# Kernel optimization log

Hardware: AMD Instinct MI355X
Metric: run time of the kernel (lower is better)

The kernel has to match this reference:

```python
import jax, jax.numpy as jnp
import numpy as np

C = 256

def setup_inputs() -> dict:
    key = jax.random.key(0)
    ks = jax.random.split(key, 7)
    s = 1.0 / np.sqrt(C)
    x = jax.random.normal(ks[0], (4, C, 64, 64), dtype=jnp.float32)
    Wq = jax.random.uniform(ks[1], (C, C), jnp.float32, -s, s)
    bq = jax.random.uniform(ks[2], (C,), jnp.float32, -s, s)
    Wk = jax.random.uniform(ks[3], (C, C), jnp.float32, -s, s)
    bk = jax.random.uniform(ks[4], (C,), jnp.float32, -s, s)
    Wv = jax.random.uniform(ks[5], (C, C), jnp.float32, -s, s)
    bv = jax.random.uniform(ks[6], (C,), jnp.float32, -s, s)
    return {"x": x, "Wq": Wq, "bq": bq, "Wk": Wk, "bk": bk, "Wv": Wv, "bv": bv}

def reference(x, Wq, bq, Wk, bk, Wv, bv):
    B, Cc, H, W = x.shape
    N = H * W
    xf = x.reshape(B, Cc, N)                      # (B, C, N)
    # 1x1 conv == channel linear: out[b,o,n] = sum_c W[o,c] x[b,c,n] + b[o]
    q = jnp.einsum('oc,bcn->bno', Wq, xf) + bq    # (B, N, C)  proj_query^T
    k = jnp.einsum('oc,bcn->bon', Wk, xf) + bk[None, :, None]  # (B, C, N)
    v = jnp.einsum('oc,bcn->bon', Wv, xf) + bv[None, :, None]  # (B, C, N)
    energy = jnp.einsum('bnc,bcm->bnm', q, k)     # (B, N, N)
    attention = jax.nn.softmax(energy, axis=-1)
    # out = V @ attention^T : out[b,c,n] = sum_m v[b,c,m] * attention[b,n,m]
    out = jnp.einsum('bcm,bnm->bcn', v, attention)
    return out.reshape(B, Cc, H, W)
```

## Files before the change

kernel.cpp:

```cpp
#include <hip/hip_runtime.h>
#include <math.h>

#define BB 4
#define CC 256
#define NN 4096

using half8 = __attribute__((ext_vector_type(8))) _Float16;
using f32x4 = __attribute__((ext_vector_type(4))) float;

__device__ __forceinline__ unsigned short f2h(float f) {
  _Float16 h = (_Float16)f;
  return __builtin_bit_cast(unsigned short, h);
}
__device__ __forceinline__ float h2f(unsigned short u) {
  return (float)__builtin_bit_cast(_Float16, u);
}

#define ASYNC16(g, l)                                                        \
  __builtin_amdgcn_global_load_lds(                                          \
      (const __attribute__((address_space(1))) unsigned int*)(g),            \
      (__attribute__((address_space(3))) unsigned int*)(l), 16, 0, 0)

__device__ __forceinline__ int row512_off(int r, int chunk) {
  return r * 256 + (((chunk & 24) | ((chunk ^ r) & 7)) << 3);
}
__device__ __forceinline__ int vt_off(int r, int chunk) {
  return r * 64 + (((chunk ^ r) & 7) << 3);
}

__global__ __launch_bounds__(512) void k_proj(const float* __restrict__ x,
    const float* __restrict__ Wq, const float* __restrict__ bq,
    const float* __restrict__ Wk, const float* __restrict__ bk,
    const float* __restrict__ Wv, const float* __restrict__ bv,
    unsigned short* __restrict__ Q, unsigned short* __restrict__ K,
    unsigned short* __restrict__ V) {
  __shared__ __align__(16) char ps[84992];
  float* xf = (float*)ps;
  unsigned short* wh = (unsigned short*)(ps + 34048);
  unsigned short* xa = (unsigned short*)(ps + 66816);
  int proj = blockIdx.z, b = blockIdx.y, n0 = blockIdx.x * 128;
  int t = threadIdx.x, w = t >> 6, lane = t & 63, l15 = lane & 15, quad = lane >> 4;
  const float* W    = proj == 0 ? Wq : (proj == 1 ? Wk : Wv);
  const float* bias = proj == 0 ? bq : (proj == 1 ? bk : bv);

  f32x4 z = {0.f, 0.f, 0.f, 0.f};
  f32x4 acc[16];
#pragma unroll
  for (int i = 0; i < 16; ++i) acc[i] = z;

  for (int ks = 0; ks < 4; ++ks) {
    if (ks) __syncthreads();
#pragma unroll
    for (int p = 0; p < 4; ++p) {
      int c = p * 16 + (t >> 5), nl = (t & 31) * 4;
      float4 v = *(const float4*)(x + ((size_t)b * CC + ks * 64 + c) * NN + n0 + nl);
      float* d = xf + c * 133 + nl;
      d[0] = v.x; d[1] = v.y; d[2] = v.z; d[3] = v.w;
    }
#pragma unroll
    for (int p = 0; p < 8; ++p) {
      int o = p * 32 + (t >> 4), c4 = (t & 15) * 4;
      float4 wv = *(const float4*)(W + (size_t)o * CC + ks * 64 + c4);
      ushort4 pk;
      pk.x = f2h(wv.x); pk.y = f2h(wv.y); pk.z = f2h(wv.z); pk.w = f2h(wv.w);
      int ch = c4 >> 3;
      *(ushort4*)&wh[o * 64 + (((ch ^ o) & 7) << 3) + (c4 & 7)] = pk;
    }
    __syncthreads();
#pragma unroll
    for (int s = 0; s < 2; ++s) {
      int n = t >> 2, cb = (t & 3) * 16 + s * 8;
      union { unsigned short u[8]; uint4 v4; } tmp;
#pragma unroll
      for (int i = 0; i < 8; ++i) tmp.u[i] = f2h(xf[(cb + i) * 133 + n]);
      *(uint4*)&xa[n * 64 + ((((cb >> 3) ^ n) & 7) << 3)] = tmp.v4;
    }
    __syncthreads();
#pragma unroll
    for (int kc = 0; kc < 2; ++kc) {
      half8 af = *(const half8*)&xa[vt_off(w * 16 + l15, kc * 4 + quad)];
#pragma unroll
      for (int ct = 0; ct < 16; ++ct) {
        half8 bf = *(const half8*)&wh[vt_off(ct * 16 + l15, kc * 4 + quad)];
        acc[ct] = __builtin_amdgcn_mfma_f32_16x16x32_f16(af, bf, acc[ct], 0, 0, 0);
      }
    }
  }
#pragma unroll
  for (int ct = 0; ct < 16; ++ct) {
    float bv_ = bias[ct * 16 + l15];
#pragma unroll
    for (int r = 0; r < 4; ++r) acc[ct][r] += bv_;
  }
  __syncthreads();
  if (proj < 2) {
    unsigned short (*qo)[264] = (unsigned short(*)[264])ps;
#pragma unroll
    for (int ct = 0; ct < 16; ++ct)
#pragma unroll
      for (int r = 0; r < 4; ++r)
        qo[w * 16 + quad * 4 + r][ct * 16 + l15] = f2h(acc[ct][r]);
    __syncthreads();
    unsigned short* outp = (proj == 0 ? Q : K) + ((size_t)b * NN + n0) * CC;
#pragma unroll
    for (int p = 0; p < 8; ++p) {
      int f = p * 8192 + t * 16;
      int n = f >> 9, off = f & 511;
      *(uint4*)((char*)outp + (size_t)n * 512 + off) =
        *(const uint4*)((const char*)&qo[n][0] + off);
    }
  } else {
    unsigned short (*vo)[132] = (unsigned short(*)[132])ps;
#pragma unroll
    for (int ct = 0; ct < 16; ++ct)
#pragma unroll
      for (int r = 0; r < 4; ++r)
        vo[ct * 16 + l15][w * 16 + quad * 4 + r] = f2h(acc[ct][r]);
    __syncthreads();
#pragma unroll
    for (int p = 0; p < 8; ++p) {
      int f = p * 8192 + t * 16;
      int o = f >> 8, off = f & 255;
      *(uint4*)((char*)V + (((size_t)b * CC + o) * NN + n0) * 2 + off) =
        *(const uint4*)((const char*)&vo[o][0] + off);
    }
  }
}

__global__ __launch_bounds__(512) void k_flash(const unsigned short* __restrict__ Q,
    const unsigned short* __restrict__ K, const unsigned short* __restrict__ V,
    float* __restrict__ out, unsigned short* __restrict__ opart,
    float* __restrict__ ml, int n_splits) {
  __shared__ unsigned short ktA[16384], ktB[16384];
  __shared__ unsigned short vt[16384];
  __shared__ unsigned short pt[8192];
  __shared__ float al[128], ll[128];
  int b = blockIdx.y, q0 = blockIdx.x * 128, split = blockIdx.z;
  int nper = 64 / n_splits;
  int t = threadIdx.x, w = t >> 6, lane = t & 63, l15 = lane & 15, quad = lane >> 4;
  int g = w >> 1, h = w & 1;

  half8 qf[8];
  const unsigned short* qrow = Q + ((size_t)b * NN + q0 + w * 16 + l15) * CC;
#pragma unroll
  for (int k = 0; k < 8; ++k) qf[k] = *(const half8*)(qrow + k * 32 + quad * 8);

  f32x4 z = {0.f, 0.f, 0.f, 0.f};
  f32x4 o_acc[2][8];
#pragma unroll
  for (int mt = 0; mt < 2; ++mt)
#pragma unroll
    for (int i = 0; i < 8; ++i) o_acc[mt][i] = z;
  float m_i[4], lp_[4];
#pragma unroll
  for (int r = 0; r < 4; ++r) { m_i[r] = -INFINITY; lp_[r] = 0.f; }

  int it_beg = split * nper, it_end = it_beg + nper;

  auto dma_k = [&](int it, unsigned short* dst) {
    const char* kb = (const char*)(K + ((size_t)b * NN + it * 64) * CC);
#pragma unroll
    for (int p = 0; p < 4; ++p) {
      int c = p * 512 + t;
      int r = c >> 5, lo = c & 31;
      int ch = (lo & 24) | ((lo ^ r) & 7);
      ASYNC16(kb + r * 512 + ch * 16, &dst[(p * 512 + (w << 6)) * 8]);
    }
  };
  auto dma_v = [&](int it) {
    const char* vb = (const char*)(V + (size_t)b * CC * NN + it * 64);
#pragma unroll
    for (int p = 0; p < 4; ++p) {
      int c = p * 512 + t;
      int r = c >> 3;
      int ch = (c ^ r) & 7;
      ASYNC16(vb + (size_t)r * 8192 + ch * 16, &vt[(p * 512 + (w << 6)) * 8]);
    }
  };

  auto body = [&](const unsigned short* cur, unsigned short* nxt, int it) {
    if (it + 1 < it_end) dma_k(it + 1, nxt);
    dma_v(it);

    f32x4 sa[4];
#pragma unroll
    for (int j = 0; j < 4; ++j) sa[j] = z;
#pragma unroll
    for (int kk = 0; kk < 8; ++kk) {
#pragma unroll
      for (int j = 0; j < 4; ++j) {
        half8 bf = *(const half8*)&cur[row512_off(j * 16 + l15, kk * 4 + quad)];
        sa[j] = __builtin_amdgcn_mfma_f32_16x16x32_f16(qf[kk], bf, sa[j], 0, 0, 0);
      }
    }
    float mt4[4];
#pragma unroll
    for (int r = 0; r < 4; ++r)
      mt4[r] = fmaxf(fmaxf(sa[0][r], sa[1][r]), fmaxf(sa[2][r], sa[3][r]));
#pragma unroll
    for (int off = 1; off < 16; off <<= 1)
#pragma unroll
      for (int r = 0; r < 4; ++r)
        mt4[r] = fmaxf(mt4[r], __shfl_xor(mt4[r], off, 64));
    float alpha[4];
#pragma unroll
    for (int r = 0; r < 4; ++r) {
      float mn = fmaxf(m_i[r], mt4[r]);
      alpha[r] = __expf(m_i[r] - mn);
      m_i[r] = mn;
    }
#pragma unroll
    for (int r = 0; r < 4; ++r) {
      float ls = 0.f;
#pragma unroll
      for (int j = 0; j < 4; ++j) {
        float p = __expf(sa[j][r] - m_i[r]);
        sa[j][r] = p;
        ls += p;
      }
      lp_[r] = lp_[r] * alpha[r] + ls;
    }
    if (l15 == 0) {
#pragma unroll
      for (int r = 0; r < 4; ++r) al[w * 16 + quad * 4 + r] = alpha[r];
    }
#pragma unroll
    for (int j = 0; j < 4; ++j)
#pragma unroll
      for (int r = 0; r < 4; ++r) {
        int row = w * 16 + quad * 4 + r;
        int ch = 2 * j + (l15 >> 3);
        pt[row * 64 + (((ch ^ row) & 7) << 3) + (l15 & 7)] = f2h(sa[j][r]);
      }
    __syncthreads();

    float a_al[2][4];
#pragma unroll
    for (int mt = 0; mt < 2; ++mt)
#pragma unroll
      for (int r = 0; r < 4; ++r)
        a_al[mt][r] = al[g * 32 + mt * 16 + quad * 4 + r];
#pragma unroll
    for (int mt = 0; mt < 2; ++mt)
#pragma unroll
      for (int ct = 0; ct < 8; ++ct)
#pragma unroll
        for (int r = 0; r < 4; ++r) o_acc[mt][ct][r] *= a_al[mt][r];
#pragma unroll
    for (int ks2 = 0; ks2 < 2; ++ks2) {
      half8 af[2];
#pragma unroll
      for (int mt = 0; mt < 2; ++mt) {
        int row_p = g * 32 + mt * 16 + l15;
        af[mt] = *(const half8*)&pt[row_p * 64 + ((((ks2 * 4 + quad) ^ row_p) & 7) << 3)];
      }
#pragma unroll
      for (int ct = 0; ct < 8; ++ct) {
        half8 bf = *(const half8*)&vt[vt_off(h * 128 + ct * 16 + l15, ks2 * 4 + quad)];
#pragma unroll
        for (int mt = 0; mt < 2; ++mt)
          o_acc[mt][ct] = __builtin_amdgcn_mfma_f32_16x16x32_f16(af[mt], bf, o_acc[mt][ct], 0, 0, 0);
      }
    }
    __syncthreads();
  };

  dma_k(it_beg, ktA);
  __syncthreads();
  for (int it = it_beg; it < it_end; it += 2) {
    body(ktA, ktB, it);
    body(ktB, ktA, it + 1);
  }

#pragma unroll
  for (int off = 1; off < 16; off <<= 1)
#pragma unroll
    for (int r = 0; r < 4; ++r)
      lp_[r] += __shfl_xor(lp_[r], off, 64);
  if (l15 == 0) {
#pragma unroll
    for (int r = 0; r < 4; ++r) ll[w * 16 + quad * 4 + r] = lp_[r];
  }
  if (n_splits != 1 && l15 == 0) {
    size_t qi = (size_t)q0 + w * 16 + quad * 4;
    float* mp = ml + ((size_t)(split * 2 + 0) * BB + b) * NN + qi;
    float* lq = ml + ((size_t)(split * 2 + 1) * BB + b) * NN + qi;
#pragma unroll
    for (int r = 0; r < 4; ++r) { mp[r] = m_i[r]; lq[r] = lp_[r]; }
  }
  __syncthreads();
  float sc[2][4];
#pragma unroll
  for (int mt = 0; mt < 2; ++mt)
#pragma unroll
    for (int r = 0; r < 4; ++r) {
      float lv = ll[g * 32 + mt * 16 + quad * 4 + r];
      sc[mt][r] = (n_splits == 1) ? 1.f / lv : 1.f;
    }

  float* od = (float*)ktA;
  float* obf = out + (size_t)b * CC * NN + q0;
  unsigned short* obh = opart + ((size_t)split * BB + b) * CC * NN + q0;
#pragma unroll
  for (int pp = 0; pp < 8; ++pp) {
    __syncthreads();
    if (h == (pp >> 2)) {
#pragma unroll
      for (int cp = 0; cp < 2; ++cp) {
        int ct = (pp & 3) * 2 + cp;
#pragma unroll
        for (int mt = 0; mt < 2; ++mt)
#pragma unroll
          for (int r = 0; r < 4; ++r)
            od[(cp * 16 + l15) * 132 + g * 32 + mt * 16 + quad * 4 + r] =
                o_acc[mt][ct][r] * sc[mt][r];
      }
    }
    __syncthreads();
    if (n_splits == 1) {
#pragma unroll
      for (int p2 = 0; p2 < 2; ++p2) {
        int row = p2 * 16 + (t >> 5);
        *(float4*)(obf + (size_t)(pp * 32 + row) * NN + (t & 31) * 4) =
          *(const float4*)&od[row * 132 + (t & 31) * 4];
      }
    } else {
      int row = t >> 4, q8 = (t & 15) * 8;
      union { unsigned short u[8]; uint4 v4; } tmp;
#pragma unroll
      for (int i2 = 0; i2 < 8; ++i2) tmp.u[i2] = f2h(od[row * 132 + q8 + i2]);
      *(uint4*)(obh + (size_t)(pp * 32 + row) * NN + q8) = tmp.v4;
    }
  }
}

__global__ __launch_bounds__(256) void k_merge(const unsigned short* __restrict__ opart,
    const float* __restrict__ ml, float* __restrict__ out) {
  size_t i = ((size_t)blockIdx.x * 256 + threadIdx.x) * 4;
  int n = (int)(i & (NN - 1));
  int b = (int)(i >> 20);
  float4 m1 = *(const float4*)(ml + ((size_t)(0 * BB) + b) * NN + n);
  float4 l1 = *(const float4*)(ml + ((size_t)(1 * BB) + b) * NN + n);
  float4 m2 = *(const float4*)(ml + ((size_t)(2 * BB) + b) * NN + n);
  float4 l2 = *(const float4*)(ml + ((size_t)(3 * BB) + b) * NN + n);
  ushort4 o1 = *(const ushort4*)(opart + i);
  ushort4 o2 = *(const ushort4*)(opart + (size_t)BB * CC * NN + i);
  float4 res;
#define MRG(f, comp) { \
    float M = fmaxf(m1.f, m2.f); \
    float e1 = __expf(m1.f - M), e2 = __expf(m2.f - M); \
    res.f = (e1 * h2f(o1.comp) + e2 * h2f(o2.comp)) / (e1 * l1.f + e2 * l2.f); }
  MRG(x, x) MRG(y, y) MRG(z, z) MRG(w, w)
#undef MRG
  *(float4*)(out + i) = res;
}

extern "C" void kernel_launch(void* const* d_in, const int* in_sizes, int n_in,
                              void* d_out, int out_size, void* d_ws, size_t ws_size,
                              hipStream_t stream) {
  const float* x  = (const float*)d_in[0];
  const float* Wq = (const float*)d_in[1];
  const float* bq = (const float*)d_in[2];
  const float* Wk = (const float*)d_in[3];
  const float* bk = (const float*)d_in[4];
  const float* Wv = (const float*)d_in[5];
  const float* bv = (const float*)d_in[6];
  float* out = (float*)d_out;
  char* ws = (char*)d_ws;
  const size_t MB = 1024 * 1024;
  unsigned short* Qb = (unsigned short*)(ws);
  unsigned short* Kb = (unsigned short*)(ws + 8 * MB);
  unsigned short* Vb = (unsigned short*)(ws + 16 * MB);
  unsigned short* Op = (unsigned short*)(ws + 24 * MB);
  float*          Ml = (float*)(ws + 40 * MB);

  k_proj<<<dim3(32, 4, 3), 512, 0, stream>>>(x, Wq, bq, Wk, bk, Wv, bv, Qb, Kb, Vb);

  int ns = (ws_size >= 41 * MB) ? 2 : 1;
  k_flash<<<dim3(32, 4, ns), 512, 0, stream>>>(Qb, Kb, Vb, out, Op, Ml, ns);
  if (ns == 2) k_merge<<<dim3(4096), 256, 0, stream>>>(Op, Ml, out);
}
```

Measured before the change: 215.1 us.

## Precast weights once and fuse Q/K/V projections into one 32-column tile kernel

A new small kernel converts all three weight matrices to fp16 in a pre-swizzled layout once per call. The projection kernel now computes Q, K and V together for a 32-column tile, so each x tile is loaded and converted once instead of three times. Weights are streamed into LDS with async global-to-LDS loads. This adds an extra launch and a larger LDS footprint (about 108 KB), which may limit occupancy, and grows the grid from 384 to 512 blocks of smaller tiles.

New measurement: 213.2 us. Within noise of the previous version (-0.9%).

```diff
diff --git a/kernel.cpp b/kernel.cpp
--- a/kernel.cpp
+++ b/kernel.cpp
@@ -28,101 +28,138 @@
   return r * 64 + (((chunk ^ r) & 7) << 3);
 }
 
+__global__ __launch_bounds__(256) void k_wcast(const float* __restrict__ Wq,
+    const float* __restrict__ Wk, const float* __restrict__ Wv,
+    unsigned short* __restrict__ Wt) {
+  int id = blockIdx.x * 256 + threadIdx.x;
+  int pos8 = id & 7, o = (id >> 3) & 255, ks = (id >> 11) & 3, p3 = id >> 13;
+  const float* W = p3 == 0 ? Wq : (p3 == 1 ? Wk : Wv);
+  int c = ks * 64 + ((pos8 ^ o) & 7) * 8;
+  const float* src = W + (size_t)o * CC + c;
+  float4 a = *(const float4*)(src);
+  float4 b4 = *(const float4*)(src + 4);
+  union { unsigned short u[8]; uint4 v4; } pk;
+  pk.u[0] = f2h(a.x);  pk.u[1] = f2h(a.y);  pk.u[2] = f2h(a.z);  pk.u[3] = f2h(a.w);
+  pk.u[4] = f2h(b4.x); pk.u[5] = f2h(b4.y); pk.u[6] = f2h(b4.z); pk.u[7] = f2h(b4.w);
+  *(uint4*)(Wt + (size_t)id * 8) = pk.v4;
+}
+
 __global__ __launch_bounds__(512) void k_proj(const float* __restrict__ x,
-    const float* __restrict__ Wq, const float* __restrict__ bq,
-    const float* __restrict__ Wk, const float* __restrict__ bk,
-    const float* __restrict__ Wv, const float* __restrict__ bv,
+    const unsigned short* __restrict__ Wt,
+    const float* __restrict__ bq, const float* __restrict__ bk,
+    const float* __restrict__ bv,
     unsigned short* __restrict__ Q, unsigned short* __restrict__ K,
     unsigned short* __restrict__ V) {
-  __shared__ __align__(16) char ps[84992];
+  __shared__ __align__(16) char ps[110848];
   float* xf = (float*)ps;
-  unsigned short* wh = (unsigned short*)(ps + 34048);
-  unsigned short* xa = (unsigned short*)(ps + 66816);
-  int proj = blockIdx.z, b = blockIdx.y, n0 = blockIdx.x * 128;
+  unsigned short* xa = (unsigned short*)(ps + 8448);
+  unsigned short* wh = (unsigned short*)(ps + 12544);
+  int b = blockIdx.y, n0 = blockIdx.x * 32;
   int t = threadIdx.x, w = t >> 6, lane = t & 63, l15 = lane & 15, quad = lane >> 4;
-  const float* W    = proj == 0 ? Wq : (proj == 1 ? Wk : Wv);
-  const float* bias = proj == 0 ? bq : (proj == 1 ? bk : bv);
 
   f32x4 z = {0.f, 0.f, 0.f, 0.f};
-  f32x4 acc[16];
-#pragma unroll
-  for (int i = 0; i < 16; ++i) acc[i] = z;
+  f32x4 acc[3][2][2];
+#pragma unroll
+  for (int p3 = 0; p3 < 3; ++p3)
+#pragma unroll
+    for (int ct = 0; ct < 2; ++ct)
+#pragma unroll
+      for (int mt = 0; mt < 2; ++mt) acc[p3][ct][mt] = z;
 
   for (int ks = 0; ks < 4; ++ks) {
     if (ks) __syncthreads();
 #pragma unroll
-    for (int p = 0; p < 4; ++p) {
-      int c = p * 16 + (t >> 5), nl = (t & 31) * 4;
+    for (int p3 = 0; p3 < 3; ++p3) {
+      const char* wb = (const char*)(Wt + (size_t)(p3 * 4 + ks) * 16384);
+#pragma unroll
+      for (int p = 0; p < 4; ++p) {
+        int c = p * 512 + t;
+        ASYNC16(wb + c * 16, &wh[p3 * 16384 + (p * 512 + (w << 6)) * 8]);
+      }
+    }
+    {
+      int c = t >> 3, nl = (t & 7) * 4;
       float4 v = *(const float4*)(x + ((size_t)b * CC + ks * 64 + c) * NN + n0 + nl);
-      float* d = xf + c * 133 + nl;
+      float* d = xf + c * 33 + nl;
       d[0] = v.x; d[1] = v.y; d[2] = v.z; d[3] = v.w;
     }
-#pragma unroll
-    for (int p = 0; p < 8; ++p) {
-      int o = p * 32 + (t >> 4), c4 = (t & 15) * 4;
-      float4 wv = *(const float4*)(W + (size_t)o * CC + ks * 64 + c4);
-      ushort4 pk;
-      pk.x = f2h(wv.x); pk.y = f2h(wv.y); pk.z = f2h(wv.z); pk.w = f2h(wv.w);
-      int ch = c4 >> 3;
-      *(ushort4*)&wh[o * 64 + (((ch ^ o) & 7) << 3) + (c4 & 7)] = pk;
-    }
-    __syncthreads();
-#pragma unroll
-    for (int s = 0; s < 2; ++s) {
-      int n = t >> 2, cb = (t & 3) * 16 + s * 8;
-      union { unsigned short u[8]; uint4 v4; } tmp;
-#pragma unroll
-      for (int i = 0; i < 8; ++i) tmp.u[i] = f2h(xf[(cb + i) * 133 + n]);
-      *(uint4*)&xa[n * 64 + ((((cb >> 3) ^ n) & 7) << 3)] = tmp.v4;
+    __syncthreads();
+    {
+      int n = t >> 4, cb = (t & 15) * 4;
+      union { unsigned short u[4]; ushort4 v4; } tmp;
+#pragma unroll
+      for (int i = 0; i < 4; ++i) tmp.u[i] = f2h(xf[(cb + i) * 33 + n]);
+      int ch = cb >> 3;
+      *(ushort4*)&xa[n * 64 + (((ch ^ n) & 7) << 3) + (cb & 7)] = tmp.v4;
     }
     __syncthreads();
 #pragma unroll
     for (int kc = 0; kc < 2; ++kc) {
-      half8 af = *(const half8*)&xa[vt_off(w * 16 + l15, kc * 4 + quad)];
-#pragma unroll
-      for (int ct = 0; ct < 16; ++ct) {
-        half8 bf = *(const half8*)&wh[vt_off(ct * 16 + l15, kc * 4 + quad)];
-        acc[ct] = __builtin_amdgcn_mfma_f32_16x16x32_f16(af, bf, acc[ct], 0, 0, 0);
-      }
-    }
-  }
-#pragma unroll
-  for (int ct = 0; ct < 16; ++ct) {
-    float bv_ = bias[ct * 16 + l15];
-#pragma unroll
-    for (int r = 0; r < 4; ++r) acc[ct][r] += bv_;
-  }
-  __syncthreads();
-  if (proj < 2) {
-    unsigned short (*qo)[264] = (unsigned short(*)[264])ps;
-#pragma unroll
-    for (int ct = 0; ct < 16; ++ct)
-#pragma unroll
-      for (int r = 0; r < 4; ++r)
-        qo[w * 16 + quad * 4 + r][ct * 16 + l15] = f2h(acc[ct][r]);
-    __syncthreads();
-    unsigned short* outp = (proj == 0 ? Q : K) + ((size_t)b * NN + n0) * CC;
-#pragma unroll
-    for (int p = 0; p < 8; ++p) {
+      half8 af[2];
+#pragma unroll
+      for (int mt = 0; mt < 2; ++mt)
+        af[mt] = *(const half8*)&xa[vt_off(mt * 16 + l15, kc * 4 + quad)];
+#pragma unroll
+      for (int p3 = 0; p3 < 3; ++p3)
+#pragma unroll
+        for (int ct = 0; ct < 2; ++ct) {
+          half8 bf = *(const half8*)&wh[p3 * 16384 + vt_off(w * 32 + ct * 16 + l15, kc * 4 + quad)];
+#pragma unroll
+          for (int mt = 0; mt < 2; ++mt)
+            acc[p3][ct][mt] = __builtin_amdgcn_mfma_f32_16x16x32_f16(af[mt], bf, acc[p3][ct][mt], 0, 0, 0);
+        }
+    }
+  }
+#pragma unroll
+  for (int p3 = 0; p3 < 3; ++p3) {
+    const float* bias = p3 == 0 ? bq : (p3 == 1 ? bk : bv);
+#pragma unroll
+    for (int ct = 0; ct < 2; ++ct) {
+      float bv_ = bias[w * 32 + ct * 16 + l15];
+#pragma unroll
+      for (int mt = 0; mt < 2; ++mt)
+#pragma unroll
+        for (int r = 0; r < 4; ++r) acc[p3][ct][mt][r] += bv_;
+    }
+  }
+#pragma unroll
+  for (int p3 = 0; p3 < 2; ++p3) {
+    __syncthreads();
+    unsigned short* qo = (unsigned short*)ps;
+#pragma unroll
+    for (int ct = 0; ct < 2; ++ct)
+#pragma unroll
+      for (int mt = 0; mt < 2; ++mt)
+#pragma unroll
+        for (int r = 0; r < 4; ++r)
+          qo[(mt * 16 + quad * 4 + r) * 264 + w * 32 + ct * 16 + l15] = f2h(acc[p3][ct][mt][r]);
+    __syncthreads();
+    unsigned short* outp = (p3 == 0 ? Q : K) + ((size_t)b * NN + n0) * CC;
+#pragma unroll
+    for (int p = 0; p < 2; ++p) {
       int f = p * 8192 + t * 16;
       int n = f >> 9, off = f & 511;
       *(uint4*)((char*)outp + (size_t)n * 512 + off) =
-        *(const uint4*)((const char*)&qo[n][0] + off);
-    }
-  } else {
-    unsigned short (*vo)[132] = (unsigned short(*)[132])ps;
-#pragma unroll
-    for (int ct = 0; ct < 16; ++ct)
-#pragma unroll
-      for (int r = 0; r < 4; ++r)
-        vo[ct * 16 + l15][w * 16 + quad * 4 + r] = f2h(acc[ct][r]);
-    __syncthreads();
-#pragma unroll
-    for (int p = 0; p < 8; ++p) {
-      int f = p * 8192 + t * 16;
-      int o = f >> 8, off = f & 255;
-      *(uint4*)((char*)V + (((size_t)b * CC + o) * NN + n0) * 2 + off) =
-        *(const uint4*)((const char*)&vo[o][0] + off);
+        *(const uint4*)((const char*)&qo[n * 264] + off);
+    }
+  }
+  {
+    __syncthreads();
+    unsigned short* vo = (unsigned short*)ps;
+#pragma unroll
+    for (int ct = 0; ct < 2; ++ct)
+#pragma unroll
+      for (int mt = 0; mt < 2; ++mt)
+#pragma unroll
+        for (int r = 0; r < 4; ++r)
+          vo[(w * 32 + ct * 16 + l15) * 36 + mt * 16 + quad * 4 + r] = f2h(acc[2][ct][mt][r]);
+    __syncthreads();
+#pragma unroll
+    for (int p = 0; p < 2; ++p) {
+      int id = p * 512 + t;
+      int o = id >> 2, off = (id & 3) * 16;
+      *(uint4*)((char*)(V + ((size_t)b * CC + o) * NN + n0) + off) =
+        *(const uint4*)((const char*)&vo[o * 36] + off);
     }
   }
 }
@@ -374,9 +411,13 @@
   unsigned short* Op = (unsigned short*)(ws + 24 * MB);
   float*          Ml = (float*)(ws + 40 * MB);
 
-  k_proj<<<dim3(32, 4, 3), 512, 0, stream>>>(x, Wq, bq, Wk, bk, Wv, bv, Qb, Kb, Vb);
-
   int ns = (ws_size >= 41 * MB) ? 2 : 1;
+  unsigned short* Wt = (unsigned short*)(ns == 2 ? ws + 40 * MB + 256 * 1024
+                                                 : ws + 24 * MB);
+
+  k_wcast<<<dim3(96), 256, 0, stream>>>(Wq, Wk, Wv, Wt);
+  k_proj<<<dim3(128, 4), 512, 0, stream>>>(x, Wt, bq, bk, bv, Qb, Kb, Vb);
+
   k_flash<<<dim3(32, 4, ns), 512, 0, stream>>>(Qb, Kb, Vb, out, Op, Ml, ns);
   if (ns == 2) k_merge<<<dim3(4096), 256, 0, stream>>>(Op, Ml, out);
 }
```
